# Kernel tuning notes

Hardware: AMD Instinct MI355X
Metric: run time of the kernel (lower is better)

Reference implementation:

```python
import math
import jax, jax.numpy as jnp
import numpy as np

N, T, D, H = 256, 128, 1024, 1024


def setup_inputs() -> dict:
    key = jax.random.key(0)
    k1, k2, k3, k4, k5 = jax.random.split(key, 5)
    x = jax.random.normal(k1, (N, T, D), dtype=jnp.float32)
    A = jax.random.normal(k2, (N, H, 4, 4), dtype=jnp.float32)
    Wx = jax.random.normal(k3, (D, 4 * H), dtype=jnp.float32) / math.sqrt(D)
    Wh = jax.random.normal(k4, (H, 4 * H), dtype=jnp.float32) / math.sqrt(H)
    Wattn = jax.random.normal(k5, (H, 4 * H), dtype=jnp.float32) / math.sqrt(H)
    b = jnp.zeros((4 * H,), dtype=jnp.float32)
    return {"x": x, "A": A, "Wx": Wx, "Wh": Wh, "Wattn": Wattn, "b": b}


def reference(x, A, Wx, Wh, Wattn, b):
    n, h = A.shape[0], A.shape[1]
    Af = A.reshape(n, h, 16)           # (N, H, 16) flattened 4x4 feature map
    h0 = Af.mean(axis=2)               # mean-pooled global feature inits h0, c0
    scale = 1.0 / math.sqrt(h)

    def step(carry, x_t):
        prev_h, prev_c = carry
        # scaled dot-product attention over 16 spatial locations
        logits = jnp.einsum("nh,nhl->nl", prev_h, Af) * scale   # (N, 16)
        w = jax.nn.softmax(logits, axis=1)
        attn = jnp.einsum("nhl,nl->nh", Af, w)                  # (N, H)
        # LSTM gates
        pre = x_t @ Wx + prev_h @ Wh + attn @ Wattn + b          # (N, 4H)
        i, f, o, g = jnp.split(pre, 4, axis=1)
        next_c = jax.nn.sigmoid(f) * prev_c + jax.nn.sigmoid(i) * jnp.tanh(g)
        next_h = jax.nn.sigmoid(o) * jnp.tanh(next_c)
        return (next_h, next_c), next_h

    xs = jnp.swapaxes(x, 0, 1)         # (T, N, D)
    _, hs = jax.lax.scan(step, (h0, h0), xs)
    return jnp.swapaxes(hs, 0, 1)      # (N, T, H)
```

## Files before the change

### kernel.cpp

```cpp
#include <hip/hip_runtime.h>
#include <hip/hip_bf16.h>

#define NB 256
#define TT 128
#define DD 1024
#define HH 1024
#define FH 4096
#define KTOT 3072

typedef __attribute__((ext_vector_type(4))) float f32x4;
typedef __attribute__((ext_vector_type(8))) short short8;

__device__ __forceinline__ unsigned short f2bf(float f) {
    union { float f; unsigned u; } v; v.f = f;
    unsigned u = v.u;
    u += 0x7FFFu + ((u >> 16) & 1u);
    return (unsigned short)(u >> 16);
}
__device__ __forceinline__ float sigm(float v) { return 1.f / (1.f + __expf(-v)); }
__device__ __forceinline__ float tanhf_(float v) { return 1.f - 2.f / (__expf(2.f * v) + 1.f); }

__device__ __forceinline__ void bmap(int bid, int& m0, int& j0) {
    int x = bid & 7, y = (bid >> 3) & 7, mt = bid >> 6;
    m0 = mt * 64;
    j0 = (x * 8 + y) * 16;
}

__global__ __launch_bounds__(256) void wt_prep(const float* __restrict__ Wx,
                                               const float* __restrict__ Wh,
                                               const float* __restrict__ Wattn,
                                               unsigned short* __restrict__ Wt) {
    __shared__ unsigned short tile[64][65];
    int k0 = blockIdx.x * 64;
    int c0 = blockIdx.y * 64;
    const float* src; int kl0;
    if (k0 < 1024)      { src = Wx;    kl0 = k0; }
    else if (k0 < 2048) { src = Wh;    kl0 = k0 - 1024; }
    else                { src = Wattn; kl0 = k0 - 2048; }
    int tid = threadIdx.x;
    int r = tid >> 2;
    int ch = (tid & 3) << 4;
    const float* p = src + (size_t)(kl0 + r) * FH + c0 + ch;
#pragma unroll
    for (int i = 0; i < 16; i += 4) {
        float4 v = *reinterpret_cast<const float4*>(p + i);
        tile[r][ch + i + 0] = f2bf(v.x);
        tile[r][ch + i + 1] = f2bf(v.y);
        tile[r][ch + i + 2] = f2bf(v.z);
        tile[r][ch + i + 3] = f2bf(v.w);
    }
    __syncthreads();
    alignas(16) unsigned short vals[16];
#pragma unroll
    for (int i = 0; i < 16; ++i) vals[i] = tile[ch + i][r];
    unsigned short* q = Wt + (size_t)(c0 + r) * KTOT + k0 + ch;
    *reinterpret_cast<uint4*>(q)     = *reinterpret_cast<uint4*>(&vals[0]);
    *reinterpret_cast<uint4*>(q + 8) = *reinterpret_cast<uint4*>(&vals[8]);
}

__global__ __launch_bounds__(256) void zero_buf(float* __restrict__ p, int n) {
    int i = blockIdx.x * 256 + threadIdx.x;
    if (i < n) p[i] = 0.f;
}

__global__ __launch_bounds__(512) void init_kernel(const float* __restrict__ A,
                                                   float* __restrict__ c,
                                                   unsigned short* __restrict__ hcat,
                                                   float* __restrict__ lg0) {
    int m0, j0; bmap(blockIdx.x, m0, j0);
    int tid = threadIdx.x;
    int r = tid >> 3, j2 = (tid & 7) * 2;
    int n = m0 + r;
    float lg[16];
#pragma unroll
    for (int l = 0; l < 16; ++l) lg[l] = 0.f;
#pragma unroll
    for (int e = 0; e < 2; ++e) {
        int j = j0 + j2 + e;
        const float4* p = reinterpret_cast<const float4*>(A + ((size_t)n * HH + j) * 16);
        float4 a0 = p[0], a1 = p[1], a2 = p[2], a3 = p[3];
        float av[16] = {a0.x,a0.y,a0.z,a0.w, a1.x,a1.y,a1.z,a1.w,
                        a2.x,a2.y,a2.z,a2.w, a3.x,a3.y,a3.z,a3.w};
        float s = 0.f;
#pragma unroll
        for (int l = 0; l < 16; ++l) s += av[l];
        float m = s * 0.0625f;
        c[(size_t)n * HH + j] = m;
        hcat[(size_t)n * 3072 + j] = f2bf(m);
#pragma unroll
        for (int l = 0; l < 16; ++l) lg[l] += m * av[l];
    }
#pragma unroll
    for (int l = 0; l < 16; ++l) {
        lg[l] += __shfl_xor(lg[l], 1);
        lg[l] += __shfl_xor(lg[l], 2);
        lg[l] += __shfl_xor(lg[l], 4);
    }
    int l0 = (tid & 7) * 2;
    atomicAdd(&lg0[(size_t)n * 16 + l0],     lg[l0]);
    atomicAdd(&lg0[(size_t)n * 16 + l0 + 1], lg[l0 + 1]);
}

__global__ __launch_bounds__(512) void attn_phase(const float* __restrict__ lgcur,
                                                  float* __restrict__ lgz,
                                                  const float* __restrict__ A,
                                                  unsigned short* __restrict__ hcat) {
    int m0, j0; bmap(blockIdx.x, m0, j0);
    int tid = threadIdx.x;
    int r = tid >> 3, j2 = (tid & 7) * 2;
    int n = m0 + r;
    const float4* lp = reinterpret_cast<const float4*>(lgcur + (size_t)n * 16);
    float4 s0 = lp[0], s1 = lp[1], s2 = lp[2], s3 = lp[3];
    float s[16] = {s0.x,s0.y,s0.z,s0.w, s1.x,s1.y,s1.z,s1.w,
                   s2.x,s2.y,s2.z,s2.w, s3.x,s3.y,s3.z,s3.w};
    float mx = -1e30f;
#pragma unroll
    for (int l = 0; l < 16; ++l) { s[l] *= 0.03125f; mx = fmaxf(mx, s[l]); }
    float wsum = 0.f;
    float w[16];
#pragma unroll
    for (int l = 0; l < 16; ++l) { w[l] = __expf(s[l] - mx); wsum += w[l]; }
    float inv = 1.f / wsum;
#pragma unroll
    for (int e = 0; e < 2; ++e) {
        int j = j0 + j2 + e;
        const float4* p = reinterpret_cast<const float4*>(A + ((size_t)n * HH + j) * 16);
        float4 a0 = p[0], a1 = p[1], a2 = p[2], a3 = p[3];
        float av[16] = {a0.x,a0.y,a0.z,a0.w, a1.x,a1.y,a1.z,a1.w,
                        a2.x,a2.y,a2.z,a2.w, a3.x,a3.y,a3.z,a3.w};
        float acc = 0.f;
#pragma unroll
        for (int l = 0; l < 16; ++l) acc += av[l] * w[l];
        hcat[(size_t)n * 3072 + 2048 + j] = f2bf(acc * inv);
    }
    if ((blockIdx.x & 63) == 0) {
        int l0 = (tid & 7) * 2;
        lgz[(size_t)n * 16 + l0]     = 0.f;
        lgz[(size_t)n * 16 + l0 + 1] = 0.f;
    }
}

__global__ __launch_bounds__(512) void gemm_fused(const float* __restrict__ x,
                                                  unsigned short* hcat,
                                                  const unsigned short* __restrict__ Wt,
                                                  const float* __restrict__ A,
                                                  const float* __restrict__ b,
                                                  float* __restrict__ c,
                                                  float* __restrict__ out,
                                                  float* __restrict__ lgnext, int t) {
    __shared__ unsigned short As[64][64];
    __shared__ unsigned short Bs[64][64];
    __shared__ float gsm[4][64][17];

    int m0, j0; bmap(blockIdx.x, m0, j0);
    int tid = threadIdx.x;
    int w = tid >> 6, lane = tid & 63;
    int gate = w & 3, kh = w >> 2;
    int hsel = t & 1;

    int srow = tid >> 3;
    int kel  = (tid & 7) << 3;
    int scol = kel ^ ((srow & 7) << 3);
    int an = m0 + srow;
    int brow = ((srow >> 4) * 1024) + j0 + (srow & 15);
    const unsigned short* bptr0 = Wt + (size_t)brow * KTOT + kel;
    const unsigned short* hrow  = hcat + (size_t)an * 3072;
    const float* xrow = x + ((size_t)an * TT + t) * DD + kel;

    uint4 ra, rb;
    auto preload = [&](int kt) {
        int k0 = kt << 6;
        if (k0 < 1024) {
            float4 v0 = *reinterpret_cast<const float4*>(xrow + k0);
            float4 v1 = *reinterpret_cast<const float4*>(xrow + k0 + 4);
            ra.x = (unsigned)f2bf(v0.x) | ((unsigned)f2bf(v0.y) << 16);
            ra.y = (unsigned)f2bf(v0.z) | ((unsigned)f2bf(v0.w) << 16);
            ra.z = (unsigned)f2bf(v1.x) | ((unsigned)f2bf(v1.y) << 16);
            ra.w = (unsigned)f2bf(v1.z) | ((unsigned)f2bf(v1.w) << 16);
        } else {
            int off = (k0 < 2048) ? (hsel * 1024 + (k0 - 1024) + kel) : (k0 + kel);
            ra = *reinterpret_cast<const uint4*>(hrow + off);
        }
        rb = *reinterpret_cast<const uint4*>(bptr0 + k0);
    };

    f32x4 acc[4];
#pragma unroll
    for (int mi = 0; mi < 4; ++mi)
#pragma unroll
        for (int e = 0; e < 4; ++e) acc[mi][e] = 0.f;

    preload(0);
    for (int kt = 0; kt < 48; ++kt) {
        if (kt) __syncthreads();
        *reinterpret_cast<uint4*>(&As[srow][scol]) = ra;
        *reinterpret_cast<uint4*>(&Bs[srow][scol]) = rb;
        if (kt + 1 < 48) preload(kt + 1);
        __syncthreads();

        int kbase = kh * 32 + ((lane >> 4) << 3);
        int fcol  = kbase ^ ((lane & 7) << 3);
        short8 bfr = *reinterpret_cast<const short8*>(&Bs[gate * 16 + (lane & 15)][fcol]);
#pragma unroll
        for (int mi = 0; mi < 4; ++mi) {
            short8 afr = *reinterpret_cast<const short8*>(&As[mi * 16 + (lane & 15)][fcol]);
            acc[mi] = __builtin_amdgcn_mfma_f32_16x16x32_bf16(afr, bfr, acc[mi], 0, 0, 0);
        }
    }

    int crow = (lane >> 4) << 2;
    int ccol = lane & 15;
    if (w < 4) {
#pragma unroll
        for (int mi = 0; mi < 4; ++mi)
#pragma unroll
            for (int e = 0; e < 4; ++e)
                gsm[gate][mi * 16 + crow + e][ccol] = acc[mi][e];
    }
    __syncthreads();
    if (w >= 4) {
#pragma unroll
        for (int mi = 0; mi < 4; ++mi)
#pragma unroll
            for (int e = 0; e < 4; ++e)
                gsm[gate][mi * 16 + crow + e][ccol] += acc[mi][e];
    }
    __syncthreads();

    int r = tid >> 3, j2 = (tid & 7) * 2;
    int n = m0 + r;
    int j = j0 + j2;
    float2 cv = *reinterpret_cast<const float2*>(c + (size_t)n * HH + j);
    float hn[2], cn[2];
#pragma unroll
    for (int e = 0; e < 2; ++e) {
        float ig = sigm(gsm[0][r][j2 + e] + b[0 * HH + j + e]);
        float fg = sigm(gsm[1][r][j2 + e] + b[1 * HH + j + e]);
        float og = sigm(gsm[2][r][j2 + e] + b[2 * HH + j + e]);
        float gg = tanhf_(gsm[3][r][j2 + e] + b[3 * HH + j + e]);
        float cc = fg * (e ? cv.y : cv.x) + ig * gg;
        cn[e] = cc;
        hn[e] = og * tanhf_(cc);
    }
    *reinterpret_cast<float2*>(c + (size_t)n * HH + j) = make_float2(cn[0], cn[1]);
    hcat[(size_t)n * 3072 + (hsel ^ 1) * 1024 + j]     = f2bf(hn[0]);
    hcat[(size_t)n * 3072 + (hsel ^ 1) * 1024 + j + 1] = f2bf(hn[1]);
    *reinterpret_cast<float2*>(out + ((size_t)n * TT + t) * HH + j) = make_float2(hn[0], hn[1]);

    float lg[16];
#pragma unroll
    for (int l = 0; l < 16; ++l) lg[l] = 0.f;
#pragma unroll
    for (int e = 0; e < 2; ++e) {
        const float4* p = reinterpret_cast<const float4*>(A + ((size_t)n * HH + j + e) * 16);
        float4 a0 = p[0], a1 = p[1], a2 = p[2], a3 = p[3];
        float av[16] = {a0.x,a0.y,a0.z,a0.w, a1.x,a1.y,a1.z,a1.w,
                        a2.x,a2.y,a2.z,a2.w, a3.x,a3.y,a3.z,a3.w};
        float hv = hn[e];
#pragma unroll
        for (int l = 0; l < 16; ++l) lg[l] += hv * av[l];
    }
#pragma unroll
    for (int l = 0; l < 16; ++l) {
        lg[l] += __shfl_xor(lg[l], 1);
        lg[l] += __shfl_xor(lg[l], 2);
        lg[l] += __shfl_xor(lg[l], 4);
    }
    int l0 = (tid & 7) * 2;
    atomicAdd(&lgnext[(size_t)n * 16 + l0],     lg[l0]);
    atomicAdd(&lgnext[(size_t)n * 16 + l0 + 1], lg[l0 + 1]);
}

extern "C" void kernel_launch(void* const* d_in, const int* in_sizes, int n_in,
                              void* d_out, int out_size, void* d_ws, size_t ws_size,
                              hipStream_t stream) {
    const float* x     = (const float*)d_in[0];
    const float* A     = (const float*)d_in[1];
    const float* Wx    = (const float*)d_in[2];
    const float* Wh    = (const float*)d_in[3];
    const float* Wattn = (const float*)d_in[4];
    const float* b     = (const float*)d_in[5];
    float* out = (float*)d_out;

    char* ws = (char*)d_ws;
    unsigned short* Wt   = (unsigned short*)(ws);
    unsigned short* hcat = (unsigned short*)(ws + 25165824);
    float* c             = (float*)(ws + 26738688);
    float* lg            = (float*)(ws + 27787264);

    wt_prep<<<dim3(48, 64), 256, 0, stream>>>(Wx, Wh, Wattn, Wt);
    zero_buf<<<48, 256, 0, stream>>>(lg, 3 * NB * 16);
    init_kernel<<<256, 512, 0, stream>>>(A, c, hcat, lg);
    for (int t = 0; t < TT; ++t) {
        attn_phase<<<256, 512, 0, stream>>>(lg + (t % 3) * NB * 16,
                                            lg + ((t + 2) % 3) * NB * 16, A, hcat);
        gemm_fused<<<256, 512, 0, stream>>>(x, hcat, Wt, A, b, c, out,
                                            lg + ((t + 1) % 3) * NB * 16, t);
    }
}
```

Measured before the change: 5.026 ms.

## Replace LDS-staged GEMM loop with per-wave split-K direct-load MFMA

The per-timestep gate GEMM no longer stages 64x64 A/B tiles through shared memory with two barriers per K-step. Each of the 8 waves instead takes a 384-wide K slice and loads its bf16 fragments straight from global memory, converting x to bf16 on the fly. Each wave computes the full 64x64 tile as a 4x4 grid of MFMAs, and the partial sums are then reduced across waves in LDS. This removes about 96 barriers per block and raises MFMA work per load, at the cost of more registers per wave (launch_bounds 512,2) and less coalesced 16-byte strided global reads.

```diff
diff --git a/kernel.cpp b/kernel.cpp
--- a/kernel.cpp
+++ b/kernel.cpp
@@ -24,6 +24,15 @@
     int x = bid & 7, y = (bid >> 3) & 7, mt = bid >> 6;
     m0 = mt * 64;
     j0 = (x * 8 + y) * 16;
+}
+
+__device__ __forceinline__ short8 pack8(float4 v0, float4 v1) {
+    short8 r;
+    r[0] = (short)f2bf(v0.x); r[1] = (short)f2bf(v0.y);
+    r[2] = (short)f2bf(v0.z); r[3] = (short)f2bf(v0.w);
+    r[4] = (short)f2bf(v1.x); r[5] = (short)f2bf(v1.y);
+    r[6] = (short)f2bf(v1.z); r[7] = (short)f2bf(v1.w);
+    return r;
 }
 
 __global__ __launch_bounds__(256) void wt_prep(const float* __restrict__ Wx,
@@ -86,7 +95,7 @@
         for (int l = 0; l < 16; ++l) s += av[l];
         float m = s * 0.0625f;
         c[(size_t)n * HH + j] = m;
-        hcat[(size_t)n * 3072 + j] = f2bf(m);
+        hcat[(size_t)n * KTOT + j] = f2bf(m);
 #pragma unroll
         for (int l = 0; l < 16; ++l) lg[l] += m * av[l];
     }
@@ -131,7 +140,7 @@
         float acc = 0.f;
 #pragma unroll
         for (int l = 0; l < 16; ++l) acc += av[l] * w[l];
-        hcat[(size_t)n * 3072 + 2048 + j] = f2bf(acc * inv);
+        hcat[(size_t)n * KTOT + 2048 + j] = f2bf(acc * inv);
     }
     if ((blockIdx.x & 63) == 0) {
         int l0 = (tid & 7) * 2;
@@ -140,90 +149,161 @@
     }
 }
 
-__global__ __launch_bounds__(512) void gemm_fused(const float* __restrict__ x,
-                                                  unsigned short* hcat,
-                                                  const unsigned short* __restrict__ Wt,
-                                                  const float* __restrict__ A,
-                                                  const float* __restrict__ b,
-                                                  float* __restrict__ c,
-                                                  float* __restrict__ out,
-                                                  float* __restrict__ lgnext, int t) {
-    __shared__ unsigned short As[64][64];
-    __shared__ unsigned short Bs[64][64];
-    __shared__ float gsm[4][64][17];
-
+template<int N>
+__device__ __forceinline__ void run_h(const unsigned short* const* ap,
+                                      const unsigned short* const* bp,
+                                      f32x4 (&acc)[4][4]) {
+#pragma unroll
+    for (int c2 = 0; c2 < N; ++c2) {
+        short8 a[4], b[4];
+#pragma unroll
+        for (int i = 0; i < 4; ++i)
+            a[i] = *reinterpret_cast<const short8*>(ap[i] + c2 * 32);
+#pragma unroll
+        for (int i = 0; i < 4; ++i)
+            b[i] = *reinterpret_cast<const short8*>(bp[i] + c2 * 32);
+#pragma unroll
+        for (int mi = 0; mi < 4; ++mi)
+#pragma unroll
+            for (int ni = 0; ni < 4; ++ni)
+                acc[mi][ni] = __builtin_amdgcn_mfma_f32_16x16x32_bf16(
+                    a[mi], b[ni], acc[mi][ni], 0, 0, 0);
+    }
+}
+
+template<int N>
+__device__ __forceinline__ void run_x(const float* const* xp,
+                                      const unsigned short* const* bp,
+                                      f32x4 (&acc)[4][4]) {
+#pragma unroll
+    for (int c2 = 0; c2 < N; ++c2) {
+        short8 a[4], b[4];
+#pragma unroll
+        for (int i = 0; i < 4; ++i) {
+            float4 v0 = *reinterpret_cast<const float4*>(xp[i] + c2 * 32);
+            float4 v1 = *reinterpret_cast<const float4*>(xp[i] + c2 * 32 + 4);
+            a[i] = pack8(v0, v1);
+        }
+#pragma unroll
+        for (int i = 0; i < 4; ++i)
+            b[i] = *reinterpret_cast<const short8*>(bp[i] + c2 * 32);
+#pragma unroll
+        for (int mi = 0; mi < 4; ++mi)
+#pragma unroll
+            for (int ni = 0; ni < 4; ++ni)
+                acc[mi][ni] = __builtin_amdgcn_mfma_f32_16x16x32_bf16(
+                    a[mi], b[ni], acc[mi][ni], 0, 0, 0);
+    }
+}
+
+__global__ __launch_bounds__(512, 2) void gemm_fused(const float* __restrict__ x,
+                                                     unsigned short* __restrict__ hcat,
+                                                     const unsigned short* __restrict__ Wt,
+                                                     const float* __restrict__ A,
+                                                     const float* __restrict__ b,
+                                                     float* __restrict__ c,
+                                                     float* __restrict__ out,
+                                                     float* __restrict__ lgnext, int t) {
+    __shared__ float red[4][64][68];
     int m0, j0; bmap(blockIdx.x, m0, j0);
     int tid = threadIdx.x;
     int w = tid >> 6, lane = tid & 63;
-    int gate = w & 3, kh = w >> 2;
     int hsel = t & 1;
-
-    int srow = tid >> 3;
-    int kel  = (tid & 7) << 3;
-    int scol = kel ^ ((srow & 7) << 3);
-    int an = m0 + srow;
-    int brow = ((srow >> 4) * 1024) + j0 + (srow & 15);
-    const unsigned short* bptr0 = Wt + (size_t)brow * KTOT + kel;
-    const unsigned short* hrow  = hcat + (size_t)an * 3072;
-    const float* xrow = x + ((size_t)an * TT + t) * DD + kel;
-
-    uint4 ra, rb;
-    auto preload = [&](int kt) {
-        int k0 = kt << 6;
-        if (k0 < 1024) {
-            float4 v0 = *reinterpret_cast<const float4*>(xrow + k0);
-            float4 v1 = *reinterpret_cast<const float4*>(xrow + k0 + 4);
-            ra.x = (unsigned)f2bf(v0.x) | ((unsigned)f2bf(v0.y) << 16);
-            ra.y = (unsigned)f2bf(v0.z) | ((unsigned)f2bf(v0.w) << 16);
-            ra.z = (unsigned)f2bf(v1.x) | ((unsigned)f2bf(v1.y) << 16);
-            ra.w = (unsigned)f2bf(v1.z) | ((unsigned)f2bf(v1.w) << 16);
-        } else {
-            int off = (k0 < 2048) ? (hsel * 1024 + (k0 - 1024) + kel) : (k0 + kel);
-            ra = *reinterpret_cast<const uint4*>(hrow + off);
-        }
-        rb = *reinterpret_cast<const uint4*>(bptr0 + k0);
-    };
-
-    f32x4 acc[4];
+    int ks = w * 384;
+    int cw = lane & 15;
+    int klane = (lane >> 4) << 3;
+
+    f32x4 acc[4][4];
 #pragma unroll
     for (int mi = 0; mi < 4; ++mi)
 #pragma unroll
-        for (int e = 0; e < 4; ++e) acc[mi][e] = 0.f;
-
-    preload(0);
-    for (int kt = 0; kt < 48; ++kt) {
-        if (kt) __syncthreads();
-        *reinterpret_cast<uint4*>(&As[srow][scol]) = ra;
-        *reinterpret_cast<uint4*>(&Bs[srow][scol]) = rb;
-        if (kt + 1 < 48) preload(kt + 1);
-        __syncthreads();
-
-        int kbase = kh * 32 + ((lane >> 4) << 3);
-        int fcol  = kbase ^ ((lane & 7) << 3);
-        short8 bfr = *reinterpret_cast<const short8*>(&Bs[gate * 16 + (lane & 15)][fcol]);
-#pragma unroll
-        for (int mi = 0; mi < 4; ++mi) {
-            short8 afr = *reinterpret_cast<const short8*>(&As[mi * 16 + (lane & 15)][fcol]);
-            acc[mi] = __builtin_amdgcn_mfma_f32_16x16x32_bf16(afr, bfr, acc[mi], 0, 0, 0);
-        }
-    }
-
-    int crow = (lane >> 4) << 2;
-    int ccol = lane & 15;
+        for (int ni = 0; ni < 4; ++ni)
+#pragma unroll
+            for (int e = 0; e < 4; ++e) acc[mi][ni][e] = 0.f;
+
+    const unsigned short* bp[4];
+#pragma unroll
+    for (int ni = 0; ni < 4; ++ni)
+        bp[ni] = Wt + (size_t)(ni * 1024 + j0 + cw) * KTOT + ks + klane;
+
+    if (w < 2) {
+        const float* xp[4];
+#pragma unroll
+        for (int mi = 0; mi < 4; ++mi)
+            xp[mi] = x + ((size_t)(m0 + mi * 16 + cw) * TT + t) * DD + ks + klane;
+        run_x<12>(xp, bp, acc);
+    } else if (w == 2) {
+        const float* xp[4];
+#pragma unroll
+        for (int mi = 0; mi < 4; ++mi)
+            xp[mi] = x + ((size_t)(m0 + mi * 16 + cw) * TT + t) * DD + ks + klane;
+        run_x<8>(xp, bp, acc);
+        const unsigned short* hp[4];
+        const unsigned short* bp2[4];
+#pragma unroll
+        for (int mi = 0; mi < 4; ++mi)
+            hp[mi] = hcat + (size_t)(m0 + mi * 16 + cw) * KTOT + hsel * 1024 + klane;
+#pragma unroll
+        for (int ni = 0; ni < 4; ++ni) bp2[ni] = bp[ni] + 256;
+        run_h<4>(hp, bp2, acc);
+    } else if (w <= 4) {
+        const unsigned short* hp[4];
+        int hoff = hsel * 1024 + (ks - 1024);
+#pragma unroll
+        for (int mi = 0; mi < 4; ++mi)
+            hp[mi] = hcat + (size_t)(m0 + mi * 16 + cw) * KTOT + hoff + klane;
+        run_h<12>(hp, bp, acc);
+    } else if (w == 5) {
+        const unsigned short* hp[4];
+#pragma unroll
+        for (int mi = 0; mi < 4; ++mi)
+            hp[mi] = hcat + (size_t)(m0 + mi * 16 + cw) * KTOT + hsel * 1024 + 896 + klane;
+        run_h<4>(hp, bp, acc);
+        const unsigned short* hp2[4];
+        const unsigned short* bp2[4];
+#pragma unroll
+        for (int mi = 0; mi < 4; ++mi)
+            hp2[mi] = hcat + (size_t)(m0 + mi * 16 + cw) * KTOT + 2048 + klane;
+#pragma unroll
+        for (int ni = 0; ni < 4; ++ni) bp2[ni] = bp[ni] + 128;
+        run_h<8>(hp2, bp2, acc);
+    } else {
+        const unsigned short* hp[4];
+#pragma unroll
+        for (int mi = 0; mi < 4; ++mi)
+            hp[mi] = hcat + (size_t)(m0 + mi * 16 + cw) * KTOT + ks + klane;
+        run_h<12>(hp, bp, acc);
+    }
+
+    int r0 = (lane >> 4) << 2;
     if (w < 4) {
 #pragma unroll
         for (int mi = 0; mi < 4; ++mi)
 #pragma unroll
-            for (int e = 0; e < 4; ++e)
-                gsm[gate][mi * 16 + crow + e][ccol] = acc[mi][e];
+            for (int ni = 0; ni < 4; ++ni)
+                *reinterpret_cast<f32x4*>(&red[w][ni * 16 + cw][mi * 16 + r0]) = acc[mi][ni];
     }
     __syncthreads();
     if (w >= 4) {
 #pragma unroll
         for (int mi = 0; mi < 4; ++mi)
 #pragma unroll
-            for (int e = 0; e < 4; ++e)
-                gsm[gate][mi * 16 + crow + e][ccol] += acc[mi][e];
+            for (int ni = 0; ni < 4; ++ni) {
+                f32x4 v = *reinterpret_cast<const f32x4*>(&red[w - 4][ni * 16 + cw][mi * 16 + r0]);
+                v += acc[mi][ni];
+                *reinterpret_cast<f32x4*>(&red[w - 4][ni * 16 + cw][mi * 16 + r0]) = v;
+            }
+    }
+    __syncthreads();
+#pragma unroll
+    for (int s = 0; s < 2; ++s) {
+        int q = tid * 2 + s;
+        int cc = q >> 4, r4 = (q & 15) << 2;
+        f32x4 sum = *reinterpret_cast<const f32x4*>(&red[0][cc][r4]);
+#pragma unroll
+        for (int p = 1; p < 4; ++p)
+            sum += *reinterpret_cast<const f32x4*>(&red[p][cc][r4]);
+        *reinterpret_cast<f32x4*>(&red[0][cc][r4]) = sum;
     }
     __syncthreads();
 
@@ -234,17 +314,17 @@
     float hn[2], cn[2];
 #pragma unroll
     for (int e = 0; e < 2; ++e) {
-        float ig = sigm(gsm[0][r][j2 + e] + b[0 * HH + j + e]);
-        float fg = sigm(gsm[1][r][j2 + e] + b[1 * HH + j + e]);
-        float og = sigm(gsm[2][r][j2 + e] + b[2 * HH + j + e]);
-        float gg = tanhf_(gsm[3][r][j2 + e] + b[3 * HH + j + e]);
+        float ig = sigm(red[0][0 * 16 + j2 + e][r] + b[0 * HH + j + e]);
+        float fg = sigm(red[0][1 * 16 + j2 + e][r] + b[1 * HH + j + e]);
+        float og = sigm(red[0][2 * 16 + j2 + e][r] + b[2 * HH + j + e]);
+        float gg = tanhf_(red[0][3 * 16 + j2 + e][r] + b[3 * HH + j + e]);
         float cc = fg * (e ? cv.y : cv.x) + ig * gg;
         cn[e] = cc;
         hn[e] = og * tanhf_(cc);
     }
     *reinterpret_cast<float2*>(c + (size_t)n * HH + j) = make_float2(cn[0], cn[1]);
-    hcat[(size_t)n * 3072 + (hsel ^ 1) * 1024 + j]     = f2bf(hn[0]);
-    hcat[(size_t)n * 3072 + (hsel ^ 1) * 1024 + j + 1] = f2bf(hn[1]);
+    hcat[(size_t)n * KTOT + (hsel ^ 1) * 1024 + j]     = f2bf(hn[0]);
+    hcat[(size_t)n * KTOT + (hsel ^ 1) * 1024 + j + 1] = f2bf(hn[1]);
     *reinterpret_cast<float2*>(out + ((size_t)n * TT + t) * HH + j) = make_float2(hn[0], hn[1]);
 
     float lg[16];
```

Result: slower. 5.821 ms (+15.8%).

## Precompute A·Wattn projection to fold attention into gates and fuse per-step kernels

Applied to the files above, without the earlier changes.

Rewrites the attention term using associativity: attn@Wattn becomes softmax weights times a precomputed per-sample G = Af^T·Wattn (N×4H×16), computed once by a new MFMA GEMM. The per-step attention kernel goes away and the step GEMM shrinks from K=3072 to K=2048. The step kernel is also restructured to read operands directly from global memory and LDS-staged h, with 4-way K split across waves and no per-k-tile syncs. x can optionally be pre-converted to bf16 when the workspace is large enough. The cost is a large G buffer (~32MB) that is read every step, plus bf16 rounding of G.

```diff
diff --git a/kernel.cpp b/kernel.cpp
--- a/kernel.cpp
+++ b/kernel.cpp
@@ -17,13 +17,25 @@
     u += 0x7FFFu + ((u >> 16) & 1u);
     return (unsigned short)(u >> 16);
 }
+__device__ __forceinline__ float bf2f(unsigned short u) {
+    union { unsigned u; float f; } v; v.u = ((unsigned)u) << 16; return v.f;
+}
 __device__ __forceinline__ float sigm(float v) { return 1.f / (1.f + __expf(-v)); }
 __device__ __forceinline__ float tanhf_(float v) { return 1.f - 2.f / (__expf(2.f * v) + 1.f); }
 
 __device__ __forceinline__ void bmap(int bid, int& m0, int& j0) {
-    int x = bid & 7, y = (bid >> 3) & 7, mt = bid >> 6;
+    int xx = bid & 7, yy = (bid >> 3) & 7, mt = bid >> 6;
     m0 = mt * 64;
-    j0 = (x * 8 + y) * 16;
+    j0 = (xx * 8 + yy) * 16;
+}
+
+__device__ __forceinline__ short8 pack8(float4 v0, float4 v1) {
+    short8 r;
+    r[0] = (short)f2bf(v0.x); r[1] = (short)f2bf(v0.y);
+    r[2] = (short)f2bf(v0.z); r[3] = (short)f2bf(v0.w);
+    r[4] = (short)f2bf(v1.x); r[5] = (short)f2bf(v1.y);
+    r[6] = (short)f2bf(v1.z); r[7] = (short)f2bf(v1.w);
+    return r;
 }
 
 __global__ __launch_bounds__(256) void wt_prep(const float* __restrict__ Wx,
@@ -63,9 +75,66 @@
     if (i < n) p[i] = 0.f;
 }
 
+__global__ __launch_bounds__(256) void xconv(const float* __restrict__ x,
+                                             unsigned short* __restrict__ xbf) {
+    size_t i = ((size_t)blockIdx.x * 256 + threadIdx.x) * 8;
+    float4 v0 = *reinterpret_cast<const float4*>(x + i);
+    float4 v1 = *reinterpret_cast<const float4*>(x + i + 4);
+    short8 p = pack8(v0, v1);
+    *reinterpret_cast<short8*>(xbf + i) = p;
+}
+
+__global__ __launch_bounds__(256) void afT_prep(const float* __restrict__ A,
+                                                unsigned short* __restrict__ AfT) {
+    int n = blockIdx.x;
+#pragma unroll
+    for (int pass = 0; pass < 4; ++pass) {
+        int hh = pass * 256 + threadIdx.x;
+        const float4* p = reinterpret_cast<const float4*>(A + ((size_t)n * HH + hh) * 16);
+        float4 a0 = p[0], a1 = p[1], a2 = p[2], a3 = p[3];
+        float av[16] = {a0.x,a0.y,a0.z,a0.w, a1.x,a1.y,a1.z,a1.w,
+                        a2.x,a2.y,a2.z,a2.w, a3.x,a3.y,a3.z,a3.w};
+#pragma unroll
+        for (int l = 0; l < 16; ++l)
+            AfT[((size_t)n * 16 + l) * HH + hh] = f2bf(av[l]);
+    }
+}
+
+__global__ __launch_bounds__(256) void g_gemm(const unsigned short* __restrict__ AfT,
+                                              const unsigned short* __restrict__ Wt,
+                                              unsigned short* __restrict__ G) {
+    int n = blockIdx.y;
+    int ct = blockIdx.x;
+    int tid = threadIdx.x;
+    int wv = tid >> 6, lane = tid & 63;
+    int cw = lane & 15, k8 = (lane >> 4) << 3;
+    const unsigned short* ap  = AfT + ((size_t)n * 16 + cw) * HH + k8;
+    const unsigned short* bp0 = Wt + (size_t)(ct * 128 + wv * 32 + cw) * KTOT + 2048 + k8;
+    const unsigned short* bp1 = Wt + (size_t)(ct * 128 + wv * 32 + 16 + cw) * KTOT + 2048 + k8;
+    f32x4 acc0, acc1;
+#pragma unroll
+    for (int e = 0; e < 4; ++e) { acc0[e] = 0.f; acc1[e] = 0.f; }
+#pragma unroll
+    for (int ch = 0; ch < 32; ++ch) {
+        short8 a  = *reinterpret_cast<const short8*>(ap  + ch * 32);
+        short8 b0 = *reinterpret_cast<const short8*>(bp0 + ch * 32);
+        short8 b1 = *reinterpret_cast<const short8*>(bp1 + ch * 32);
+        acc0 = __builtin_amdgcn_mfma_f32_16x16x32_bf16(a, b0, acc0, 0, 0, 0);
+        acc1 = __builtin_amdgcn_mfma_f32_16x16x32_bf16(a, b1, acc1, 0, 0, 0);
+    }
+    int r0 = (lane >> 4) << 2;
+    int c0 = ct * 128 + wv * 32 + cw;
+#pragma unroll
+    for (int e = 0; e < 4; ++e) {
+        int l = r0 + e;
+        G[((size_t)n * FH + c0) * 16 + l]      = f2bf(acc0[e]);
+        G[((size_t)n * FH + c0 + 16) * 16 + l] = f2bf(acc1[e]);
+    }
+}
+
 __global__ __launch_bounds__(512) void init_kernel(const float* __restrict__ A,
                                                    float* __restrict__ c,
-                                                   unsigned short* __restrict__ hcat,
+                                                   unsigned short* __restrict__ h0,
                                                    float* __restrict__ lg0) {
     int m0, j0; bmap(blockIdx.x, m0, j0);
     int tid = threadIdx.x;
@@ -86,7 +155,7 @@
         for (int l = 0; l < 16; ++l) s += av[l];
         float m = s * 0.0625f;
         c[(size_t)n * HH + j] = m;
-        hcat[(size_t)n * 3072 + j] = f2bf(m);
+        h0[(size_t)n * HH + j] = f2bf(m);
 #pragma unroll
         for (int l = 0; l < 16; ++l) lg[l] += m * av[l];
     }
@@ -101,151 +170,197 @@
     atomicAdd(&lg0[(size_t)n * 16 + l0 + 1], lg[l0 + 1]);
 }
 
-__global__ __launch_bounds__(512) void attn_phase(const float* __restrict__ lgcur,
-                                                  float* __restrict__ lgz,
-                                                  const float* __restrict__ A,
-                                                  unsigned short* __restrict__ hcat) {
+template<bool XBF>
+__global__ __launch_bounds__(512)
+void gemm_step(const float* __restrict__ x, const unsigned short* __restrict__ xbf,
+               const unsigned short* __restrict__ hprev, unsigned short* __restrict__ hnext,
+               const unsigned short* __restrict__ Wt, const unsigned short* __restrict__ G,
+               const float* __restrict__ A, const float* __restrict__ bb,
+               const float* __restrict__ lgcur, float* __restrict__ lgnext,
+               float* __restrict__ lgz, float* __restrict__ c,
+               float* __restrict__ out, int t) {
+    __shared__ __attribute__((aligned(16))) char smem[131072];
+    unsigned short* hsm = reinterpret_cast<unsigned short*>(smem);
+    float* gsm = reinterpret_cast<float*>(smem);
+
     int m0, j0; bmap(blockIdx.x, m0, j0);
     int tid = threadIdx.x;
+    int w = tid >> 6, lane = tid & 63;
+    int wn = w & 1, wk = w >> 1;
+
+    {
+        int r = tid >> 3;
+        const unsigned short* hp = hprev + (size_t)(m0 + r) * HH;
+#pragma unroll
+        for (int i = 0; i < 16; ++i) {
+            int chunk = (tid & 7) + i * 8;
+            int sw = chunk ^ (r & 7);
+            *reinterpret_cast<uint4*>(&hsm[r * 1024 + sw * 8]) =
+                *reinterpret_cast<const uint4*>(hp + chunk * 8);
+        }
+    }
+    __syncthreads();
+
+    int cw = lane & 15;
+    int k8 = (lane >> 4) << 3;
+
+    f32x4 acc[4][2];
+#pragma unroll
+    for (int mf = 0; mf < 4; ++mf)
+#pragma unroll
+        for (int fn = 0; fn < 2; ++fn)
+#pragma unroll
+            for (int e = 0; e < 4; ++e) acc[mf][fn][e] = 0.f;
+
+    const unsigned short* bp[2];
+#pragma unroll
+    for (int fn = 0; fn < 2; ++fn) {
+        int col = wn * 32 + fn * 16 + cw;
+        int brow = (col >> 4) * 1024 + j0 + (col & 15);
+        int kbase = (wk < 2) ? (wk * 512) : (1024 + (wk - 2) * 512);
+        bp[fn] = Wt + (size_t)brow * KTOT + kbase + k8;
+    }
+
+    if (wk < 2) {
+        if (XBF) {
+            const unsigned short* ap[4];
+#pragma unroll
+            for (int mf = 0; mf < 4; ++mf)
+                ap[mf] = xbf + ((size_t)(m0 + mf * 16 + cw) * TT + t) * DD + wk * 512 + k8;
+#pragma unroll
+            for (int ch = 0; ch < 16; ++ch) {
+                short8 b0 = *reinterpret_cast<const short8*>(bp[0] + ch * 32);
+                short8 b1 = *reinterpret_cast<const short8*>(bp[1] + ch * 32);
+#pragma unroll
+                for (int mf = 0; mf < 4; ++mf) {
+                    short8 a = *reinterpret_cast<const short8*>(ap[mf] + ch * 32);
+                    acc[mf][0] = __builtin_amdgcn_mfma_f32_16x16x32_bf16(a, b0, acc[mf][0], 0, 0, 0);
+                    acc[mf][1] = __builtin_amdgcn_mfma_f32_16x16x32_bf16(a, b1, acc[mf][1], 0, 0, 0);
+                }
+            }
+        } else {
+            const float* ap[4];
+#pragma unroll
+            for (int mf = 0; mf < 4; ++mf)
+                ap[mf] = x + ((size_t)(m0 + mf * 16 + cw) * TT + t) * DD + wk * 512 + k8;
+#pragma unroll
+            for (int ch = 0; ch < 16; ++ch) {
+                short8 b0 = *reinterpret_cast<const short8*>(bp[0] + ch * 32);
+                short8 b1 = *reinterpret_cast<const short8*>(bp[1] + ch * 32);
+#pragma unroll
+                for (int mf = 0; mf < 4; ++mf) {
+                    float4 v0 = *reinterpret_cast<const float4*>(ap[mf] + ch * 32);
+                    float4 v1 = *reinterpret_cast<const float4*>(ap[mf] + ch * 32 + 4);
+                    short8 a = pack8(v0, v1);
+                    acc[mf][0] = __builtin_amdgcn_mfma_f32_16x16x32_bf16(a, b0, acc[mf][0], 0, 0, 0);
+                    acc[mf][1] = __builtin_amdgcn_mfma_f32_16x16x32_bf16(a, b1, acc[mf][1], 0, 0, 0);
+                }
+            }
+        }
+    } else {
+        int kq = (wk - 2) * 512;
+        int chunkBase = (kq + k8) >> 3;
+#pragma unroll
+        for (int ch = 0; ch < 16; ++ch) {
+            short8 b0 = *reinterpret_cast<const short8*>(bp[0] + ch * 32);
+            short8 b1 = *reinterpret_cast<const short8*>(bp[1] + ch * 32);
+            int chunkI = chunkBase + ch * 4;
+#pragma unroll
+            for (int mf = 0; mf < 4; ++mf) {
+                int row = mf * 16 + cw;
+                int sw = chunkI ^ (row & 7);
+                short8 a = *reinterpret_cast<const short8*>(&hsm[row * 1024 + sw * 8]);
+                acc[mf][0] = __builtin_amdgcn_mfma_f32_16x16x32_bf16(a, b0, acc[mf][0], 0, 0, 0);
+                acc[mf][1] = __builtin_amdgcn_mfma_f32_16x16x32_bf16(a, b1, acc[mf][1], 0, 0, 0);
+            }
+        }
+    }
+
+    __syncthreads();
+    int r0 = (lane >> 4) << 2;
+#pragma unroll
+    for (int mf = 0; mf < 4; ++mf)
+#pragma unroll
+        for (int fn = 0; fn < 2; ++fn)
+#pragma unroll
+            for (int e = 0; e < 4; ++e)
+                gsm[((size_t)wk * 64 + mf * 16 + r0 + e) * 68 + wn * 32 + fn * 16 + cw] =
+                    acc[mf][fn][e];
+    __syncthreads();
+
     int r = tid >> 3, j2 = (tid & 7) * 2;
     int n = m0 + r;
-    const float4* lp = reinterpret_cast<const float4*>(lgcur + (size_t)n * 16);
-    float4 s0 = lp[0], s1 = lp[1], s2 = lp[2], s3 = lp[3];
-    float s[16] = {s0.x,s0.y,s0.z,s0.w, s1.x,s1.y,s1.z,s1.w,
-                   s2.x,s2.y,s2.z,s2.w, s3.x,s3.y,s3.z,s3.w};
-    float mx = -1e30f;
-#pragma unroll
-    for (int l = 0; l < 16; ++l) { s[l] *= 0.03125f; mx = fmaxf(mx, s[l]); }
-    float wsum = 0.f;
-    float w[16];
-#pragma unroll
-    for (int l = 0; l < 16; ++l) { w[l] = __expf(s[l] - mx); wsum += w[l]; }
-    float inv = 1.f / wsum;
+
+    float sm[16];
+    {
+        const float4* lp = reinterpret_cast<const float4*>(lgcur + (size_t)n * 16);
+        float4 s0 = lp[0], s1 = lp[1], s2 = lp[2], s3 = lp[3];
+        float s[16] = {s0.x,s0.y,s0.z,s0.w, s1.x,s1.y,s1.z,s1.w,
+                       s2.x,s2.y,s2.z,s2.w, s3.x,s3.y,s3.z,s3.w};
+        float mx = -1e30f;
+#pragma unroll
+        for (int l = 0; l < 16; ++l) { s[l] *= 0.03125f; mx = fmaxf(mx, s[l]); }
+        float sum = 0.f;
+#pragma unroll
+        for (int l = 0; l < 16; ++l) { sm[l] = __expf(s[l] - mx); sum += sm[l]; }
+        float inv = 1.f / sum;
+#pragma unroll
+        for (int l = 0; l < 16; ++l) sm[l] *= inv;
+    }
+
+    float pre[4][2];
+#pragma unroll
+    for (int g = 0; g < 4; ++g)
+#pragma unroll
+        for (int e = 0; e < 2; ++e) {
+            int colL = g * 16 + j2 + e;
+            float p = gsm[((size_t)0 * 64 + r) * 68 + colL]
+                    + gsm[((size_t)1 * 64 + r) * 68 + colL]
+                    + gsm[((size_t)2 * 64 + r) * 68 + colL]
+                    + gsm[((size_t)3 * 64 + r) * 68 + colL];
+            p += bb[g * HH + j0 + j2 + e];
+            const unsigned short* gp = G + ((size_t)n * FH + g * HH + j0 + j2 + e) * 16;
+            uint4 g0 = *reinterpret_cast<const uint4*>(gp);
+            uint4 g1 = *reinterpret_cast<const uint4*>(gp + 8);
+            const unsigned* gu = reinterpret_cast<const unsigned*>(&g0);
+            float d = 0.f;
+#pragma unroll
+            for (int q = 0; q < 4; ++q) {
+                d += sm[q * 2]     * bf2f((unsigned short)(gu[q] & 0xFFFF));
+                d += sm[q * 2 + 1] * bf2f((unsigned short)(gu[q] >> 16));
+            }
+            const unsigned* gv = reinterpret_cast<const unsigned*>(&g1);
+#pragma unroll
+            for (int q = 0; q < 4; ++q) {
+                d += sm[8 + q * 2]     * bf2f((unsigned short)(gv[q] & 0xFFFF));
+                d += sm[8 + q * 2 + 1] * bf2f((unsigned short)(gv[q] >> 16));
+            }
+            pre[g][e] = p + d;
+        }
+
+    int j = j0 + j2;
+    float2 cv = *reinterpret_cast<const float2*>(c + (size_t)n * HH + j);
+    float hn[2], cn[2];
 #pragma unroll
     for (int e = 0; e < 2; ++e) {
-        int j = j0 + j2 + e;
-        const float4* p = reinterpret_cast<const float4*>(A + ((size_t)n * HH + j) * 16);
-        float4 a0 = p[0], a1 = p[1], a2 = p[2], a3 = p[3];
-        float av[16] = {a0.x,a0.y,a0.z,a0.w, a1.x,a1.y,a1.z,a1.w,
-                        a2.x,a2.y,a2.z,a2.w, a3.x,a3.y,a3.z,a3.w};
-        float acc = 0.f;
-#pragma unroll
-        for (int l = 0; l < 16; ++l) acc += av[l] * w[l];
-        hcat[(size_t)n * 3072 + 2048 + j] = f2bf(acc * inv);
-    }
+        float ig = sigm(pre[0][e]);
+        float fg = sigm(pre[1][e]);
+        float og = sigm(pre[2][e]);
+        float gg = tanhf_(pre[3][e]);
+        float cc = fg * (e ? cv.y : cv.x) + ig * gg;
+        cn[e] = cc;
+        hn[e] = og * tanhf_(cc);
+    }
+    *reinterpret_cast<float2*>(c + (size_t)n * HH + j) = make_float2(cn[0], cn[1]);
+    unsigned hpack = (unsigned)f2bf(hn[0]) | ((unsigned)f2bf(hn[1]) << 16);
+    *reinterpret_cast<unsigned*>(hnext + (size_t)n * HH + j) = hpack;
+    *reinterpret_cast<float2*>(out + ((size_t)n * TT + t) * HH + j) = make_float2(hn[0], hn[1]);
+
     if ((blockIdx.x & 63) == 0) {
         int l0 = (tid & 7) * 2;
         lgz[(size_t)n * 16 + l0]     = 0.f;
         lgz[(size_t)n * 16 + l0 + 1] = 0.f;
     }
-}
-
-__global__ __launch_bounds__(512) void gemm_fused(const float* __restrict__ x,
-                                                  unsigned short* hcat,
-                                                  const unsigned short* __restrict__ Wt,
-                                                  const float* __restrict__ A,
-                                                  const float* __restrict__ b,
-                                                  float* __restrict__ c,
-                                                  float* __restrict__ out,
-                                                  float* __restrict__ lgnext, int t) {
-    __shared__ unsigned short As[64][64];
-    __shared__ unsigned short Bs[64][64];
-    __shared__ float gsm[4][64][17];
-
-    int m0, j0; bmap(blockIdx.x, m0, j0);
-    int tid = threadIdx.x;
-    int w = tid >> 6, lane = tid & 63;
-    int gate = w & 3, kh = w >> 2;
-    int hsel = t & 1;
-
-    int srow = tid >> 3;
-    int kel  = (tid & 7) << 3;
-    int scol = kel ^ ((srow & 7) << 3);
-    int an = m0 + srow;
-    int brow = ((srow >> 4) * 1024) + j0 + (srow & 15);
-    const unsigned short* bptr0 = Wt + (size_t)brow * KTOT + kel;
-    const unsigned short* hrow  = hcat + (size_t)an * 3072;
-    const float* xrow = x + ((size_t)an * TT + t) * DD + kel;
-
-    uint4 ra, rb;
-    auto preload = [&](int kt) {
-        int k0 = kt << 6;
-        if (k0 < 1024) {
-            float4 v0 = *reinterpret_cast<const float4*>(xrow + k0);
-            float4 v1 = *reinterpret_cast<const float4*>(xrow + k0 + 4);
-            ra.x = (unsigned)f2bf(v0.x) | ((unsigned)f2bf(v0.y) << 16);
-            ra.y = (unsigned)f2bf(v0.z) | ((unsigned)f2bf(v0.w) << 16);
-            ra.z = (unsigned)f2bf(v1.x) | ((unsigned)f2bf(v1.y) << 16);
-            ra.w = (unsigned)f2bf(v1.z) | ((unsigned)f2bf(v1.w) << 16);
-        } else {
-            int off = (k0 < 2048) ? (hsel * 1024 + (k0 - 1024) + kel) : (k0 + kel);
-            ra = *reinterpret_cast<const uint4*>(hrow + off);
-        }
-        rb = *reinterpret_cast<const uint4*>(bptr0 + k0);
-    };
-
-    f32x4 acc[4];
-#pragma unroll
-    for (int mi = 0; mi < 4; ++mi)
-#pragma unroll
-        for (int e = 0; e < 4; ++e) acc[mi][e] = 0.f;
-
-    preload(0);
-    for (int kt = 0; kt < 48; ++kt) {
-        if (kt) __syncthreads();
-        *reinterpret_cast<uint4*>(&As[srow][scol]) = ra;
-        *reinterpret_cast<uint4*>(&Bs[srow][scol]) = rb;
-        if (kt + 1 < 48) preload(kt + 1);
-        __syncthreads();
-
-        int kbase = kh * 32 + ((lane >> 4) << 3);
-        int fcol  = kbase ^ ((lane & 7) << 3);
-        short8 bfr = *reinterpret_cast<const short8*>(&Bs[gate * 16 + (lane & 15)][fcol]);
-#pragma unroll
-        for (int mi = 0; mi < 4; ++mi) {
-            short8 afr = *reinterpret_cast<const short8*>(&As[mi * 16 + (lane & 15)][fcol]);
-            acc[mi] = __builtin_amdgcn_mfma_f32_16x16x32_bf16(afr, bfr, acc[mi], 0, 0, 0);
-        }
-    }
-
-    int crow = (lane >> 4) << 2;
-    int ccol = lane & 15;
-    if (w < 4) {
-#pragma unroll
-        for (int mi = 0; mi < 4; ++mi)
-#pragma unroll
-            for (int e = 0; e < 4; ++e)
-                gsm[gate][mi * 16 + crow + e][ccol] = acc[mi][e];
-    }
-    __syncthreads();
-    if (w >= 4) {
-#pragma unroll
-        for (int mi = 0; mi < 4; ++mi)
-#pragma unroll
-            for (int e = 0; e < 4; ++e)
-                gsm[gate][mi * 16 + crow + e][ccol] += acc[mi][e];
-    }
-    __syncthreads();
-
-    int r = tid >> 3, j2 = (tid & 7) * 2;
-    int n = m0 + r;
-    int j = j0 + j2;
-    float2 cv = *reinterpret_cast<const float2*>(c + (size_t)n * HH + j);
-    float hn[2], cn[2];
-#pragma unroll
-    for (int e = 0; e < 2; ++e) {
-        float ig = sigm(gsm[0][r][j2 + e] + b[0 * HH + j + e]);
-        float fg = sigm(gsm[1][r][j2 + e] + b[1 * HH + j + e]);
-        float og = sigm(gsm[2][r][j2 + e] + b[2 * HH + j + e]);
-        float gg = tanhf_(gsm[3][r][j2 + e] + b[3 * HH + j + e]);
-        float cc = fg * (e ? cv.y : cv.x) + ig * gg;
-        cn[e] = cc;
-        hn[e] = og * tanhf_(cc);
-    }
-    *reinterpret_cast<float2*>(c + (size_t)n * HH + j) = make_float2(cn[0], cn[1]);
-    hcat[(size_t)n * 3072 + (hsel ^ 1) * 1024 + j]     = f2bf(hn[0]);
-    hcat[(size_t)n * 3072 + (hsel ^ 1) * 1024 + j + 1] = f2bf(hn[1]);
-    *reinterpret_cast<float2*>(out + ((size_t)n * TT + t) * HH + j) = make_float2(hn[0], hn[1]);
 
     float lg[16];
 #pragma unroll
@@ -284,17 +399,32 @@
 
     char* ws = (char*)d_ws;
     unsigned short* Wt   = (unsigned short*)(ws);
-    unsigned short* hcat = (unsigned short*)(ws + 25165824);
-    float* c             = (float*)(ws + 26738688);
-    float* lg            = (float*)(ws + 27787264);
+    unsigned short* G    = (unsigned short*)(ws + 25165824);
+    unsigned short* AfT  = (unsigned short*)(ws + 58720256);
+    unsigned short* hbuf = (unsigned short*)(ws + 67108864);
+    float* c             = (float*)(ws + 68157440);
+    float* lg            = (float*)(ws + 69206016);
+    unsigned short* xbf  = (unsigned short*)(ws + 69255168);
+    bool use_xbf = ws_size >= (size_t)69255168 + 67108864;
 
     wt_prep<<<dim3(48, 64), 256, 0, stream>>>(Wx, Wh, Wattn, Wt);
     zero_buf<<<48, 256, 0, stream>>>(lg, 3 * NB * 16);
-    init_kernel<<<256, 512, 0, stream>>>(A, c, hcat, lg);
+    afT_prep<<<NB, 256, 0, stream>>>(A, AfT);
+    g_gemm<<<dim3(32, NB), 256, 0, stream>>>(AfT, Wt, G);
+    init_kernel<<<256, 512, 0, stream>>>(A, c, hbuf, lg);
+    if (use_xbf) xconv<<<16384, 256, 0, stream>>>(x, xbf);
+
     for (int t = 0; t < TT; ++t) {
-        attn_phase<<<256, 512, 0, stream>>>(lg + (t % 3) * NB * 16,
-                                            lg + ((t + 2) % 3) * NB * 16, A, hcat);
-        gemm_fused<<<256, 512, 0, stream>>>(x, hcat, Wt, A, b, c, out,
-                                            lg + ((t + 1) % 3) * NB * 16, t);
-    }
-}
+        const unsigned short* hp = hbuf + (size_t)(t & 1) * NB * HH;
+        unsigned short* hx       = hbuf + (size_t)((t & 1) ^ 1) * NB * HH;
+        float* lgc = lg + (size_t)(t % 3) * NB * 16;
+        float* lgn = lg + (size_t)((t + 1) % 3) * NB * 16;
+        float* lgzz = lg + (size_t)((t + 2) % 3) * NB * 16;
+        if (use_xbf)
+            gemm_step<true><<<256, 512, 0, stream>>>(x, xbf, hp, hx, Wt, G, A, b,
+                                                     lgc, lgn, lgzz, c, out, t);
+        else
+            gemm_step<false><<<256, 512, 0, stream>>>(x, xbf, hp, hx, Wt, G, A, b,
+                                                      lgc, lgn, lgzz, c, out, t);
+    }
+}
```

Result: faster. 4.220 ms (-16.0%).
